# Kernel optimization log

Hardware: AMD Instinct MI355X
Metric: run time of the kernel (lower is better)

## Reference

```python
import jax, jax.numpy as jnp
import numpy as np
import math

WS = (8, 8)        # window_size
SHIFT = (4, 4)     # shift_size
HEADS = 12
C_DIM = 384


def _rel_position_bias(cpb_w1, cpb_b1, cpb_w2):
    ws0, ws1 = WS
    # continuous relative coords table, shape (2*ws0-1, 2*ws1-1, 2)
    ch = jnp.arange(-(ws0 - 1), ws0, dtype=jnp.float32)
    cw = jnp.arange(-(ws1 - 1), ws1, dtype=jnp.float32)
    table = jnp.stack(jnp.meshgrid(ch, cw, indexing='ij'), axis=-1)
    table = table / jnp.array([ws0 - 1, ws1 - 1], jnp.float32) * 8.0
    table = jnp.sign(table) * jnp.log2(jnp.abs(table) + 1.0) / 3.0
    # cpb MLP: 2 -> 512 -> HEADS (no bias on second layer)
    h = jax.nn.relu(table @ cpb_w1.T + cpb_b1)
    bias_table = (h @ cpb_w2.T).reshape(-1, HEADS)  # ((2ws0-1)*(2ws1-1), H)
    # static relative position index (numpy, shapes are static)
    coords = np.stack(np.meshgrid(np.arange(ws0), np.arange(ws1), indexing='ij'))
    coords = coords.reshape(2, -1)
    rel = (coords[:, :, None] - coords[:, None, :]).transpose(1, 2, 0)
    rel[..., 0] += ws0 - 1
    rel[..., 1] += ws1 - 1
    rel[..., 0] *= 2 * ws1 - 1
    idx = jnp.asarray(rel.sum(-1))  # (L, L)
    bias = bias_table[idx]          # (L, L, HEADS)
    bias = jnp.transpose(bias, (2, 0, 1))  # (HEADS, L, L)
    return 16.0 * jax.nn.sigmoid(bias)


def _shift_attn_mask(pad_H, pad_W):
    ws0, ws1 = WS
    s0, s1 = SHIFT
    m = np.zeros((pad_H, pad_W), dtype=np.float32)
    cnt = 0
    h_slices = ((0, pad_H - ws0), (pad_H - ws0, pad_H - s0), (pad_H - s0, pad_H))
    w_slices = ((0, pad_W - ws1), (pad_W - ws1, pad_W - s1), (pad_W - s1, pad_W))
    for h0, h1 in h_slices:
        for w0, w1 in w_slices:
            m[h0:h1, w0:w1] = cnt
            cnt += 1
    m = m.reshape(pad_H // ws0, ws0, pad_W // ws1, ws1)
    m = m.transpose(0, 2, 1, 3).reshape(-1, ws0 * ws1)  # (nW, L)
    diff = m[:, None, :] - m[:, :, None]
    mask = np.where(diff != 0, -100.0, 0.0).astype(np.float32)
    return jnp.asarray(mask)  # (nW, L, L)


def setup_inputs() -> dict:
    key = jax.random.key(0)
    ks = jax.random.split(key, 7)
    C = C_DIM
    x = jax.random.normal(ks[0], (16, 64, 64, C), jnp.float32)
    qkv_w = jax.random.normal(ks[1], (3 * C, C), jnp.float32) * 0.02
    qkv_b = jax.random.normal(ks[2], (3 * C,), jnp.float32) * 0.02
    proj_w = jax.random.normal(ks[3], (C, C), jnp.float32) * 0.02
    proj_b = jax.random.normal(ks[4], (C,), jnp.float32) * 0.02
    logit_scale = jnp.full((HEADS, 1, 1), math.log(10.0), jnp.float32)
    cpb_w1 = jax.random.normal(ks[5], (512, 2), jnp.float32) * 0.02
    cpb_b1 = jnp.zeros((512,), jnp.float32)
    cpb_w2 = jax.random.normal(ks[6], (HEADS, 512), jnp.float32) * 0.02
    return {"x": x, "qkv_w": qkv_w, "qkv_b": qkv_b, "proj_w": proj_w,
            "proj_b": proj_b, "logit_scale": logit_scale,
            "cpb_w1": cpb_w1, "cpb_b1": cpb_b1, "cpb_w2": cpb_w2}


def reference(x, qkv_w, qkv_b, proj_w, proj_b, logit_scale, cpb_w1, cpb_b1, cpb_w2):
    B, H, W, C = x.shape
    ws0, ws1 = WS
    s0, s1 = SHIFT
    L = ws0 * ws1
    hd = C // HEADS
    # H, W are divisible by window -> no padding; shift stays nonzero
    bias = _rel_position_bias(cpb_w1, cpb_b1, cpb_w2)  # (HEADS, L, L)
    xr = jnp.roll(x, (-s0, -s1), axis=(1, 2))
    nWh, nWw = H // ws0, W // ws1
    nW = nWh * nWw
    # window partition -> (B*nW, L, C)
    xw = xr.reshape(B, nWh, ws0, nWw, ws1, C).transpose(0, 1, 3, 2, 4, 5)
    xw = xw.reshape(B * nW, L, C)
    # qkv with the k-bias zeroed (SwinV2 convention)
    qb = qkv_b.at[C:2 * C].set(0.0)
    qkv = xw @ qkv_w.T + qb
    qkv = qkv.reshape(B * nW, L, 3, HEADS, hd).transpose(2, 0, 3, 1, 4)
    q, k, v = qkv[0], qkv[1], qkv[2]  # each (B*nW, HEADS, L, hd)
    # cosine attention
    qn = q / jnp.maximum(jnp.linalg.norm(q, axis=-1, keepdims=True), 1e-12)
    kn = k / jnp.maximum(jnp.linalg.norm(k, axis=-1, keepdims=True), 1e-12)
    scale = jnp.exp(jnp.minimum(logit_scale, math.log(100.0)))  # (HEADS,1,1)
    attn = jnp.einsum('whid,whjd->whij', qn, kn) * scale + bias
    # shifted-window mask
    mask = _shift_attn_mask(H, W)  # (nW, L, L)
    attn = attn.reshape(B, nW, HEADS, L, L) + mask[None, :, None]
    attn = jax.nn.softmax(attn.reshape(B * nW, HEADS, L, L), axis=-1)
    out = jnp.einsum('whij,whjd->whid', attn, v)
    out = out.transpose(0, 2, 1, 3).reshape(B * nW, L, C)
    out = out @ proj_w.T + proj_b
    # window reverse
    out = out.reshape(B, nWh, nWw, ws0, ws1, C).transpose(0, 1, 3, 2, 4, 5)
    out = out.reshape(B, H, W, C)
    out = jnp.roll(out, (s0, s1), axis=(1, 2))
    return out
```

## Files before the change

kernel.cpp:

```cpp
#include <hip/hip_runtime.h>
#include <cstdint>
#include <cstddef>

typedef unsigned short u16;
typedef __attribute__((ext_vector_type(8))) short s16x8;
typedef __attribute__((ext_vector_type(4))) float f32x4;

#define DEV static __device__ __forceinline__

constexpr int C = 384;
constexpr int HEADS = 12;
constexpr int NQKV = 3 * C;
constexpr int TOK = 16 * 64 * 64;

constexpr size_t OFF_QKVW = 0;
constexpr size_t OFF_PROJW = OFF_QKVW + (size_t)NQKV * C * 2;
constexpr size_t OFF_BIAS  = OFF_PROJW + (size_t)C * C * 2;
constexpr size_t OFF_XG    = OFF_BIAS + (size_t)HEADS * 64 * 64 * 4;
constexpr size_t OFF_QN    = OFF_XG + (size_t)TOK * C * 2;
constexpr size_t OFF_KN    = OFF_QN + (size_t)TOK * C * 2;
constexpr size_t OFF_VT    = OFF_KN + (size_t)TOK * C * 2;
constexpr size_t OFF_MLP   = OFF_VT + (size_t)TOK * C * 2;
constexpr size_t OFF_AO    = OFF_XG;

DEV u16 f2bf(float f) {
  union { float f; uint32_t u; } v; v.f = f;
  uint32_t r = v.u + 0x7FFFu + ((v.u >> 16) & 1u);
  return (u16)(r >> 16);
}

DEV float bf2f(short h) {
  union { uint32_t u; float f; } v; v.u = ((uint32_t)(u16)h) << 16;
  return v.f;
}

DEV void async16(const u16* g, u16* l) {
  __builtin_amdgcn_global_load_lds((const __attribute__((address_space(1))) uint32_t*)g,
                                   (__attribute__((address_space(3))) uint32_t*)l, 16, 0, 0);
}

__global__ __launch_bounds__(256) void prep_kernel(
    const float* __restrict__ x, const float* __restrict__ qkv_w,
    const float* __restrict__ proj_w, u16* __restrict__ wq,
    u16* __restrict__ wp, u16* __restrict__ xg) {
  int idx = blockIdx.x * 256 + threadIdx.x;
  constexpr int QW = NQKV * C / 8;
  constexpr int PW = C * C / 8;
  const float* src;
  u16* dst;
  if (idx < QW) {
    src = qkv_w + (size_t)idx * 8; dst = wq + (size_t)idx * 8;
  } else if (idx < QW + PW) {
    int i = idx - QW;
    src = proj_w + (size_t)i * 8; dst = wp + (size_t)i * 8;
  } else {
    int i = idx - QW - PW;
    int r = i / 48, c8 = i % 48;
    int b = r >> 12, w = (r >> 6) & 63, t = r & 63;
    int y  = ((w >> 3) * 8 + (t >> 3) + 4) & 63;
    int xc = ((w & 7) * 8 + (t & 7) + 4) & 63;
    src = x + (((size_t)(b * 64 + y)) * 64 + xc) * C + c8 * 8;
    dst = xg + (size_t)r * C + (size_t)c8 * 8;
  }
  float4 a = ((const float4*)src)[0];
  float4 bq = ((const float4*)src)[1];
  union { u16 h[8]; uint4 v; } o;
  o.h[0] = f2bf(a.x);  o.h[1] = f2bf(a.y);  o.h[2] = f2bf(a.z);  o.h[3] = f2bf(a.w);
  o.h[4] = f2bf(bq.x); o.h[5] = f2bf(bq.y); o.h[6] = f2bf(bq.z); o.h[7] = f2bf(bq.w);
  *(uint4*)dst = o.v;
}

__global__ __launch_bounds__(256) void bias_mlp_kernel(
    const float* __restrict__ w1, const float* __restrict__ b1,
    const float* __restrict__ w2, float* __restrict__ mlp_out) {
  const int gid = blockIdx.x * 256 + threadIdx.x;
  if (gid >= 225 * 12) return;
  const int pt = gid / 12, q = gid % 12;
  const int a = pt / 15, b = pt % 15;
  const float dy = (float)(a - 7) * (8.f / 7.f);
  const float dx = (float)(b - 7) * (8.f / 7.f);
  const float t0 = copysignf(log2f(fabsf(dy) + 1.f) * (1.f / 3.f), dy);
  const float t1 = copysignf(log2f(fabsf(dx) + 1.f) * (1.f / 3.f), dx);
  float acc = 0.f;
  for (int j = 0; j < 512; ++j) {
    const float hh = fmaxf(w1[2 * j] * t0 + w1[2 * j + 1] * t1 + b1[j], 0.f);
    acc += hh * w2[q * 512 + j];
  }
  mlp_out[gid] = acc;
}

__global__ __launch_bounds__(256) void bias_expand_kernel(
    const float* __restrict__ mlp_out, float* __restrict__ biasf) {
  const int o = blockIdx.x * 256 + threadIdx.x;
  const int j = o & 63, i = (o >> 6) & 63, h = o >> 12;
  const int e = ((i >> 3) - (j >> 3) + 7) * 15 + ((i & 7) - (j & 7) + 7);
  const float v = mlp_out[e * 12 + h];
  biasf[o] = 16.f / (1.f + __expf(-v));
}

__global__ __launch_bounds__(256, 4) void qkv_kernel(
    const u16* __restrict__ xg, const u16* __restrict__ wq,
    const float* __restrict__ qkv_b,
    u16* __restrict__ qn, u16* __restrict__ kn, u16* __restrict__ vt) {
  __shared__ __attribute__((aligned(16))) u16 smem[4][128 * 32];
  const int tid = threadIdx.x, lane = tid & 63, wid = tid >> 6;
  const int bid = blockIdx.x;
  const int swz = (bid & 7) * 576 + (bid >> 3);
  const int n_blk = swz % 9, m_blk = swz / 9;
  const int m0 = m_blk * 128, n0 = n_blk * 128;
  const int wm = wid >> 1, wn = wid & 1;

  auto stage = [&](int buf, int t) {
    const int k0 = t * 32;
    #pragma unroll
    for (int it = 0; it < 2; ++it) {
      const int c = it * 256 + tid;
      const int rr = c >> 3;
      const int qx = (c & 7) ^ (rr & 7);
      const int r = (rr << 1) + (qx >> 2);
      const int g = qx & 3;
      async16(xg + (size_t)(m0 + r) * C + k0 + g * 8, &smem[buf][c * 8]);
      async16(wq + (size_t)(n0 + r) * C + k0 + g * 8, &smem[2 + buf][c * 8]);
    }
  };
  auto ldfrag = [&](const u16* base, int row, int g) -> s16x8 {
    const int rr = row >> 1;
    const int pos = (((row & 1) << 2) + g) ^ (rr & 7);
    return *(const s16x8*)((const char*)base + rr * 128 + pos * 16);
  };

  f32x4 acc[4][4];
  #pragma unroll
  for (int i = 0; i < 4; ++i)
    #pragma unroll
    for (int j = 0; j < 4; ++j) acc[i][j] = f32x4{0.f, 0.f, 0.f, 0.f};

  stage(0, 0);
  for (int t = 0; t < 12; ++t) {
    const int buf = t & 1;
    asm volatile("s_waitcnt vmcnt(0)" ::: "memory");
    __syncthreads();
    if (t < 11) stage(buf ^ 1, t + 1);
    s16x8 af[4], bf[4];
    const int g = lane >> 4;
    #pragma unroll
    for (int mi = 0; mi < 4; ++mi) {
      af[mi] = ldfrag(smem[buf],     wm * 64 + mi * 16 + (lane & 15), g);
      bf[mi] = ldfrag(smem[2 + buf], wn * 64 + mi * 16 + (lane & 15), g);
    }
    #pragma unroll
    for (int mi = 0; mi < 4; ++mi)
      #pragma unroll
      for (int ni = 0; ni < 4; ++ni)
        acc[mi][ni] = __builtin_amdgcn_mfma_f32_16x16x32_bf16(af[mi], bf[ni], acc[mi][ni], 0, 0, 0);
  }

  const int sec = n0 / C;
  const int colbase = n0 + wn * 64;
  float qb[4];
  #pragma unroll
  for (int ni = 0; ni < 4; ++ni)
    qb[ni] = (sec == 1) ? 0.f : qkv_b[colbase + ni * 16 + (lane & 15)];

  if (sec < 2) {
    u16* const base = (sec == 0) ? qn : kn;
    const int hb = (colbase % C) >> 5;
    #pragma unroll
    for (int mi = 0; mi < 4; ++mi) {
      #pragma unroll
      for (int r = 0; r < 4; ++r) {
        const int grow = m0 + wm * 64 + mi * 16 + ((lane >> 4) << 2) + r;
        const int w = grow >> 6, t_ = grow & 63;
        u16* dst0 = base + ((size_t)(w * 12 + hb) * 64 + t_) * 32 + (lane & 15);
        u16* dst1 = base + ((size_t)(w * 12 + hb + 1) * 64 + t_) * 32 + (lane & 15);
        dst0[0]  = f2bf(acc[mi][0][r] + qb[0]);
        dst0[16] = f2bf(acc[mi][1][r] + qb[1]);
        dst1[0]  = f2bf(acc[mi][2][r] + qb[2]);
        dst1[16] = f2bf(acc[mi][3][r] + qb[3]);
      }
    }
  } else {
    __syncthreads();
    u16* tr = &smem[0][0] + wid * 4096;
    #pragma unroll
    for (int ni = 0; ni < 4; ++ni) {
      const int dl = ni * 16 + (lane & 15);
      #pragma unroll
      for (int mi = 0; mi < 4; ++mi) {
        const int t0 = mi * 16 + ((lane >> 4) << 2);
        union { u16 h[4]; uint2 u; } pk;
        #pragma unroll
        for (int r = 0; r < 4; ++r) pk.h[r] = f2bf(acc[mi][ni][r] + qb[ni]);
        const int byte = dl * 128 + (((t0 >> 3) ^ (dl & 7)) << 4) + ((t0 & 7) << 1);
        *(uint2*)((char*)tr + byte) = pk.u;
      }
    }
    const int w_ = (m0 + wm * 64) >> 6;
    const int hbase = (colbase % C) >> 5;
    #pragma unroll
    for (int i = 0; i < 8; ++i) {
      const int d = i * 8 + (lane >> 3);
      const int tg = lane & 7;
      const int byte = d * 128 + ((tg ^ (d & 7)) << 4);
      const uint4 val = *(const uint4*)((const char*)tr + byte);
      const int head = hbase + (d >> 5), din = d & 31;
      *(uint4*)(vt + (((size_t)(w_ * 12 + head) * 32 + din) * 64 + tg * 8)) = val;
    }
  }
}

__global__ __launch_bounds__(256, 4) void attn_kernel(
    const u16* __restrict__ qn, const u16* __restrict__ kn, const u16* __restrict__ vt,
    const float* __restrict__ ls, const float* __restrict__ biasf, u16* __restrict__ ao) {
  __shared__ __attribute__((aligned(16))) u16 strip_s[4][4096];
  const int tid = threadIdx.x, lane = tid & 63, wv = tid >> 6;
  char* strip = (char*)strip_s[wv];
  const int gid = blockIdx.x * 4 + wv;
  const int w = gid / 12, h = gid - w * 12;
  const int win = w & 63, wy = win >> 3, wx = win & 7;
  const int l15 = lane & 15, qrt = lane >> 4;
  const f32x4 z4 = {0.f, 0.f, 0.f, 0.f};

  const u16* qh = qn + (size_t)gid * 2048;
  const u16* kh = kn + (size_t)gid * 2048;
  const u16* vh = vt + (size_t)gid * 2048;
  const float sc = __expf(fminf(ls[h], 4.605170185988091f));

  s16x8 aq[4], bk[4];
  #pragma unroll
  for (int mi = 0; mi < 4; ++mi)
    aq[mi] = *(const s16x8*)(qh + (mi * 16 + l15) * 32 + qrt * 8);
  #pragma unroll
  for (int ni = 0; ni < 4; ++ni)
    bk[ni] = *(const s16x8*)(kh + (ni * 16 + l15) * 32 + qrt * 8);
  #pragma unroll
  for (int mi = 0; mi < 4; ++mi) {
    float f[8]; float ss = 0.f;
    #pragma unroll
    for (int e = 0; e < 8; ++e) { f[e] = bf2f(aq[mi][e]); ss = fmaf(f[e], f[e], ss); }
    ss += __shfl_xor(ss, 16); ss += __shfl_xor(ss, 32);
    const float rn = sc / fmaxf(sqrtf(ss), 1e-12f);
    #pragma unroll
    for (int e = 0; e < 8; ++e) aq[mi][e] = (short)f2bf(f[e] * rn);
  }
  #pragma unroll
  for (int ni = 0; ni < 4; ++ni) {
    float f[8]; float ss = 0.f;
    #pragma unroll
    for (int e = 0; e < 8; ++e) { f[e] = bf2f(bk[ni][e]); ss = fmaf(f[e], f[e], ss); }
    ss += __shfl_xor(ss, 16); ss += __shfl_xor(ss, 32);
    const float rn = 1.f / fmaxf(sqrtf(ss), 1e-12f);
    #pragma unroll
    for (int e = 0; e < 8; ++e) bk[ni][e] = (short)f2bf(f[e] * rn);
  }

  f32x4 acc[4][4];
  #pragma unroll
  for (int mi = 0; mi < 4; ++mi)
    #pragma unroll
    for (int ni = 0; ni < 4; ++ni)
      acc[mi][ni] = __builtin_amdgcn_mfma_f32_16x16x32_bf16(aq[mi], bk[ni], z4, 0, 0, 0);

  int ccls[4];
  #pragma unroll
  for (int ni = 0; ni < 4; ++ni) {
    const int j = ni * 16 + l15;
    const int gy = wy * 8 + (j >> 3), gx = wx * 8 + (j & 7);
    ccls[ni] = ((gy < 56 ? 0 : (gy < 60 ? 1 : 2)) << 2) | (gx < 56 ? 0 : (gx < 60 ? 1 : 2));
  }

  #pragma unroll
  for (int mi = 0; mi < 4; ++mi) {
    #pragma unroll
    for (int r = 0; r < 4; ++r) {
      const int i = mi * 16 + qrt * 4 + r;
      const int gy = wy * 8 + (i >> 3), gx = wx * 8 + (i & 7);
      const int rcl = ((gy < 56 ? 0 : (gy < 60 ? 1 : 2)) << 2) | (gx < 56 ? 0 : (gx < 60 ? 1 : 2));
      const float* brow = biasf + ((h << 6) + i) * 64 + l15;
      float mx = -3e38f;
      #pragma unroll
      for (int ni = 0; ni < 4; ++ni) {
        float val = acc[mi][ni][r] + brow[ni * 16];
        if (rcl != ccls[ni]) val -= 100.f;
        acc[mi][ni][r] = val;
        mx = fmaxf(mx, val);
      }
      mx = fmaxf(mx, __shfl_xor(mx, 1));
      mx = fmaxf(mx, __shfl_xor(mx, 2));
      mx = fmaxf(mx, __shfl_xor(mx, 4));
      mx = fmaxf(mx, __shfl_xor(mx, 8));
      float sum = 0.f;
      #pragma unroll
      for (int ni = 0; ni < 4; ++ni) {
        const float pv = __expf(acc[mi][ni][r] - mx);
        acc[mi][ni][r] = pv; sum += pv;
      }
      sum += __shfl_xor(sum, 1); sum += __shfl_xor(sum, 2);
      sum += __shfl_xor(sum, 4); sum += __shfl_xor(sum, 8);
      const float inv = 1.f / sum;
      #pragma unroll
      for (int ni = 0; ni < 4; ++ni) {
        const int j2 = (ni * 16 + l15) * 2;
        *(u16*)(strip + i * 128 + (j2 ^ ((i & 7) << 4))) = f2bf(acc[mi][ni][r] * inv);
      }
    }
  }

  s16x8 pa[4][2];
  #pragma unroll
  for (int ni2 = 0; ni2 < 4; ++ni2) {
    const int t = ni2 * 16 + l15;
    #pragma unroll
    for (int kk = 0; kk < 2; ++kk) {
      const int j2 = (kk * 32 + qrt * 8) * 2;
      pa[ni2][kk] = *(const s16x8*)(strip + t * 128 + (j2 ^ ((t & 7) << 4)));
    }
  }
  f32x4 o2[2][4];
  #pragma unroll
  for (int mi2 = 0; mi2 < 2; ++mi2) {
    #pragma unroll
    for (int ni2 = 0; ni2 < 4; ++ni2) o2[mi2][ni2] = z4;
    #pragma unroll
    for (int kk = 0; kk < 2; ++kk) {
      const s16x8 va = *(const s16x8*)(vh + (mi2 * 16 + l15) * 64 + kk * 32 + qrt * 8);
      #pragma unroll
      for (int ni2 = 0; ni2 < 4; ++ni2)
        o2[mi2][ni2] = __builtin_amdgcn_mfma_f32_16x16x32_bf16(va, pa[ni2][kk], o2[mi2][ni2], 0, 0, 0);
    }
  }
  #pragma unroll
  for (int mi2 = 0; mi2 < 2; ++mi2) {
    #pragma unroll
    for (int ni2 = 0; ni2 < 4; ++ni2) {
      const int t = ni2 * 16 + l15;
      #pragma unroll
      for (int rp = 0; rp < 2; ++rp) {
        const int d0 = mi2 * 16 + qrt * 4 + rp * 2;
        union { u16 h2[2]; uint32_t u; } pk;
        pk.h2[0] = f2bf(o2[mi2][ni2][rp * 2]);
        pk.h2[1] = f2bf(o2[mi2][ni2][rp * 2 + 1]);
        *(uint32_t*)(strip + t * 128 + ((d0 * 2) ^ ((t & 7) << 4))) = pk.u;
      }
    }
  }
  u16* aob = ao + ((size_t)h * TOK + (size_t)w * 64) * 32;
  #pragma unroll
  for (int it = 0; it < 4; ++it) {
    const int t = (lane >> 2) + it * 16, g = lane & 3;
    const uint4 val = *(const uint4*)(strip + t * 128 + ((g * 16) ^ ((t & 7) << 4)));
    *(uint4*)(aob + (size_t)t * 32 + g * 8) = val;
  }
}

__global__ __launch_bounds__(256, 4) void proj_kernel(
    const u16* __restrict__ ao, const u16* __restrict__ pw,
    const float* __restrict__ proj_b, float* __restrict__ out) {
  __shared__ __attribute__((aligned(16))) u16 smem[4][128 * 32];
  const int tid = threadIdx.x, lane = tid & 63, wid = tid >> 6;
  const int bid = blockIdx.x;
  const int swz = (bid & 7) * 192 + (bid >> 3);
  const int n_blk = swz % 3, m_blk = swz / 3;
  const int m0 = m_blk * 128, n0 = n_blk * 128;
  const int wm = wid >> 1, wn = wid & 1;

  auto stage = [&](int buf, int t) {
    const int k0 = t * 32;
    #pragma unroll
    for (int it = 0; it < 2; ++it) {
      const int c = it * 256 + tid;
      const int rr = c >> 3;
      const int qx = (c & 7) ^ (rr & 7);
      const int r = (rr << 1) + (qx >> 2);
      const int g = qx & 3;
      async16(ao + ((size_t)t * TOK + (m0 + r)) * 32 + g * 8, &smem[buf][c * 8]);
      async16(pw + (size_t)(n0 + r) * C + k0 + g * 8, &smem[2 + buf][c * 8]);
    }
  };
  auto ldfrag = [&](const u16* base, int row, int g) -> s16x8 {
    const int rr = row >> 1;
    const int pos = (((row & 1) << 2) + g) ^ (rr & 7);
    return *(const s16x8*)((const char*)base + rr * 128 + pos * 16);
  };

  f32x4 acc[4][4];
  #pragma unroll
  for (int i = 0; i < 4; ++i)
    #pragma unroll
    for (int j = 0; j < 4; ++j) acc[i][j] = f32x4{0.f, 0.f, 0.f, 0.f};

  stage(0, 0);
  for (int t = 0; t < 12; ++t) {
    const int buf = t & 1;
    asm volatile("s_waitcnt vmcnt(0)" ::: "memory");
    __syncthreads();
    if (t < 11) stage(buf ^ 1, t + 1);
    s16x8 af[4], bf[4];
    const int g = lane >> 4;
    #pragma unroll
    for (int mi = 0; mi < 4; ++mi) {
      af[mi] = ldfrag(smem[buf],     wm * 64 + mi * 16 + (lane & 15), g);
      bf[mi] = ldfrag(smem[2 + buf], wn * 64 + mi * 16 + (lane & 15), g);
    }
    #pragma unroll
    for (int mi = 0; mi < 4; ++mi)
      #pragma unroll
      for (int ni = 0; ni < 4; ++ni)
        acc[mi][ni] = __builtin_amdgcn_mfma_f32_16x16x32_bf16(af[mi], bf[ni], acc[mi][ni], 0, 0, 0);
  }

  #pragma unroll
  for (int ni = 0; ni < 4; ++ni) {
    const int n = n0 + wn * 64 + ni * 16 + (lane & 15);
    const float pb = proj_b[n];
    #pragma unroll
    for (int mi = 0; mi < 4; ++mi) {
      #pragma unroll
      for (int r = 0; r < 4; ++r) {
        const int grow = m0 + wm * 64 + mi * 16 + ((lane >> 4) << 2) + r;
        const int bimg = grow >> 12, win = (grow >> 6) & 63, t_ = grow & 63;
        const int y = ((win >> 3) * 8 + (t_ >> 3) + 4) & 63;
        const int xc = ((win & 7) * 8 + (t_ & 7) + 4) & 63;
        out[(((size_t)bimg * 64 + y) * 64 + xc) * C + n] = acc[mi][ni][r] + pb;
      }
    }
  }
}

extern "C" void kernel_launch(void* const* d_in, const int* in_sizes, int n_in,
                              void* d_out, int out_size, void* d_ws, size_t ws_size,
                              hipStream_t stream) {
  const float* x           = (const float*)d_in[0];
  const float* qkv_w       = (const float*)d_in[1];
  const float* qkv_b       = (const float*)d_in[2];
  const float* proj_w      = (const float*)d_in[3];
  const float* proj_b      = (const float*)d_in[4];
  const float* logit_scale = (const float*)d_in[5];
  const float* cpb_w1      = (const float*)d_in[6];
  const float* cpb_b1      = (const float*)d_in[7];
  const float* cpb_w2      = (const float*)d_in[8];
  char* ws = (char*)d_ws;
  u16* qkvwb  = (u16*)(ws + OFF_QKVW);
  u16* projwb = (u16*)(ws + OFF_PROJW);
  float* biasf = (float*)(ws + OFF_BIAS);
  u16* xg = (u16*)(ws + OFF_XG);
  u16* qn = (u16*)(ws + OFF_QN);
  u16* kn = (u16*)(ws + OFF_KN);
  u16* vt = (u16*)(ws + OFF_VT);
  float* mlp = (float*)(ws + OFF_MLP);
  u16* ao = (u16*)(ws + OFF_AO);

  prep_kernel<<<12576, 256, 0, stream>>>(x, qkv_w, proj_w, qkvwb, projwb, xg);
  bias_mlp_kernel<<<11, 256, 0, stream>>>(cpb_w1, cpb_b1, cpb_w2, mlp);
  bias_expand_kernel<<<192, 256, 0, stream>>>(mlp, biasf);
  qkv_kernel<<<4608, 256, 0, stream>>>(xg, qkvwb, qkv_b, qn, kn, vt);
  attn_kernel<<<3072, 256, 0, stream>>>(qn, kn, vt, logit_scale, biasf, ao);
  proj_kernel<<<1536, 256, 0, stream>>>(ao, projwb, proj_b, (float*)d_out);
}
```

Before: 247.2 us.

## Fuse shifted-window gather and bf16 conversion of x into QKV GEMM loads

The prep kernel no longer gathers and converts the whole fp32 input into a bf16 windowed buffer. The QKV GEMM now computes the roll/window-partition addresses itself, loads fp32 x through registers, converts to bf16 and writes it to shared memory, while weights keep using async global-to-LDS loads. This removes one full read and write pass over the large activation tensor and a large kernel launch. In exchange the GEMM reads fp32 (twice the bytes) and re-reads each A tile for all nine N blocks, relying on cache reuse, and adds register pressure and conversion work inside the main loop.

Result: slower. 272.3 us (+10.2%).

```diff
diff --git a/kernel.cpp b/kernel.cpp
--- a/kernel.cpp
+++ b/kernel.cpp
@@ -40,27 +40,17 @@
 }
 
 __global__ __launch_bounds__(256) void prep_kernel(
-    const float* __restrict__ x, const float* __restrict__ qkv_w,
-    const float* __restrict__ proj_w, u16* __restrict__ wq,
-    u16* __restrict__ wp, u16* __restrict__ xg) {
+    const float* __restrict__ qkv_w, const float* __restrict__ proj_w,
+    u16* __restrict__ wq, u16* __restrict__ wp) {
   int idx = blockIdx.x * 256 + threadIdx.x;
   constexpr int QW = NQKV * C / 8;
-  constexpr int PW = C * C / 8;
   const float* src;
   u16* dst;
   if (idx < QW) {
     src = qkv_w + (size_t)idx * 8; dst = wq + (size_t)idx * 8;
-  } else if (idx < QW + PW) {
+  } else {
     int i = idx - QW;
     src = proj_w + (size_t)i * 8; dst = wp + (size_t)i * 8;
-  } else {
-    int i = idx - QW - PW;
-    int r = i / 48, c8 = i % 48;
-    int b = r >> 12, w = (r >> 6) & 63, t = r & 63;
-    int y  = ((w >> 3) * 8 + (t >> 3) + 4) & 63;
-    int xc = ((w & 7) * 8 + (t & 7) + 4) & 63;
-    src = x + (((size_t)(b * 64 + y)) * 64 + xc) * C + c8 * 8;
-    dst = xg + (size_t)r * C + (size_t)c8 * 8;
   }
   float4 a = ((const float4*)src)[0];
   float4 bq = ((const float4*)src)[1];
@@ -99,7 +89,7 @@
 }
 
 __global__ __launch_bounds__(256, 4) void qkv_kernel(
-    const u16* __restrict__ xg, const u16* __restrict__ wq,
+    const float* __restrict__ x, const u16* __restrict__ wq,
     const float* __restrict__ qkv_b,
     u16* __restrict__ qn, u16* __restrict__ kn, u16* __restrict__ vt) {
   __shared__ __attribute__((aligned(16))) u16 smem[4][128 * 32];
@@ -110,18 +100,51 @@
   const int m0 = m_blk * 128, n0 = n_blk * 128;
   const int wm = wid >> 1, wn = wid & 1;
 
-  auto stage = [&](int buf, int t) {
-    const int k0 = t * 32;
+  const float* arow[2];
+  int adst[2];
+  const u16* brow[2];
+  int bdst[2];
+  #pragma unroll
+  for (int it = 0; it < 2; ++it) {
+    const int c = it * 256 + tid;
+    const int rr = c >> 3;
+    const int qx = (c & 7) ^ (rr & 7);
+    const int r = (rr << 1) + (qx >> 2);
+    const int g = qx & 3;
+    const int grow = m0 + r;
+    const int b = grow >> 12, w = (grow >> 6) & 63, tk = grow & 63;
+    const int y  = ((w >> 3) * 8 + (tk >> 3) + 4) & 63;
+    const int xc = ((w & 7) * 8 + (tk & 7) + 4) & 63;
+    arow[it] = x + (((size_t)(b * 64 + y)) * 64 + xc) * C + g * 8;
+    adst[it] = c * 8;
+    brow[it] = wq + (size_t)(n0 + r) * C + g * 8;
+    bdst[it] = c * 8;
+  }
+
+  float4 areg[2][2];
+  auto a_load = [&](int t) {
     #pragma unroll
     for (int it = 0; it < 2; ++it) {
-      const int c = it * 256 + tid;
-      const int rr = c >> 3;
-      const int qx = (c & 7) ^ (rr & 7);
-      const int r = (rr << 1) + (qx >> 2);
-      const int g = qx & 3;
-      async16(xg + (size_t)(m0 + r) * C + k0 + g * 8, &smem[buf][c * 8]);
-      async16(wq + (size_t)(n0 + r) * C + k0 + g * 8, &smem[2 + buf][c * 8]);
-    }
+      const float* p = arow[it] + t * 32;
+      areg[it][0] = ((const float4*)p)[0];
+      areg[it][1] = ((const float4*)p)[1];
+    }
+  };
+  auto a_write = [&](int buf) {
+    #pragma unroll
+    for (int it = 0; it < 2; ++it) {
+      union { u16 h[8]; uint4 v; } o;
+      o.h[0] = f2bf(areg[it][0].x); o.h[1] = f2bf(areg[it][0].y);
+      o.h[2] = f2bf(areg[it][0].z); o.h[3] = f2bf(areg[it][0].w);
+      o.h[4] = f2bf(areg[it][1].x); o.h[5] = f2bf(areg[it][1].y);
+      o.h[6] = f2bf(areg[it][1].z); o.h[7] = f2bf(areg[it][1].w);
+      *(uint4*)(&smem[buf][adst[it]]) = o.v;
+    }
+  };
+  auto b_stage = [&](int buf, int t) {
+    #pragma unroll
+    for (int it = 0; it < 2; ++it)
+      async16(brow[it] + t * 32, &smem[2 + buf][bdst[it]]);
   };
   auto ldfrag = [&](const u16* base, int row, int g) -> s16x8 {
     const int rr = row >> 1;
@@ -135,12 +158,12 @@
     #pragma unroll
     for (int j = 0; j < 4; ++j) acc[i][j] = f32x4{0.f, 0.f, 0.f, 0.f};
 
-  stage(0, 0);
+  a_load(0); b_stage(0, 0); a_write(0);
   for (int t = 0; t < 12; ++t) {
     const int buf = t & 1;
     asm volatile("s_waitcnt vmcnt(0)" ::: "memory");
     __syncthreads();
-    if (t < 11) stage(buf ^ 1, t + 1);
+    if (t < 11) { a_load(t + 1); b_stage(buf ^ 1, t + 1); }
     s16x8 af[4], bf[4];
     const int g = lane >> 4;
     #pragma unroll
@@ -153,6 +176,7 @@
       #pragma unroll
       for (int ni = 0; ni < 4; ++ni)
         acc[mi][ni] = __builtin_amdgcn_mfma_f32_16x16x32_bf16(af[mi], bf[ni], acc[mi][ni], 0, 0, 0);
+    if (t < 11) a_write(buf ^ 1);
   }
 
   const int sec = n0 / C;
@@ -443,17 +467,16 @@
   u16* qkvwb  = (u16*)(ws + OFF_QKVW);
   u16* projwb = (u16*)(ws + OFF_PROJW);
   float* biasf = (float*)(ws + OFF_BIAS);
-  u16* xg = (u16*)(ws + OFF_XG);
   u16* qn = (u16*)(ws + OFF_QN);
   u16* kn = (u16*)(ws + OFF_KN);
   u16* vt = (u16*)(ws + OFF_VT);
   float* mlp = (float*)(ws + OFF_MLP);
   u16* ao = (u16*)(ws + OFF_AO);
 
-  prep_kernel<<<12576, 256, 0, stream>>>(x, qkv_w, proj_w, qkvwb, projwb, xg);
+  prep_kernel<<<288, 256, 0, stream>>>(qkv_w, proj_w, qkvwb, projwb);
   bias_mlp_kernel<<<11, 256, 0, stream>>>(cpb_w1, cpb_b1, cpb_w2, mlp);
   bias_expand_kernel<<<192, 256, 0, stream>>>(mlp, biasf);
-  qkv_kernel<<<4608, 256, 0, stream>>>(xg, qkvwb, qkv_b, qn, kn, vt);
+  qkv_kernel<<<4608, 256, 0, stream>>>(x, qkvwb, qkv_b, qn, kn, vt);
   attn_kernel<<<3072, 256, 0, stream>>>(qn, kn, vt, logit_scale, biasf, ao);
   proj_kernel<<<1536, 256, 0, stream>>>(ao, projwb, proj_b, (float*)d_out);
 }
```
